# Kernel optimization log

Measured on AMD Instinct MI355X. Metric: run time of the kernel, lower is better.

## Reference

```python
import jax, jax.numpy as jnp
import numpy as np

N, IN_DIM, HID, HEADS, OUT_DIM = 50000, 128, 32, 4, 64
E, P = 800000, 500000
BN_EPS = 1e-5
NEG_SLOPE = 0.2


def setup_inputs() -> dict:
    key = jax.random.key(0)
    ks = jax.random.split(key, 16)
    inp = {
        "x": jax.random.normal(ks[0], (N, IN_DIM), jnp.float32),
        "ei": jax.random.randint(ks[1], (2, E), 0, N, jnp.int64),
        "src": jax.random.randint(ks[2], (P,), 0, N, jnp.int64),
        "dst": jax.random.randint(ks[3], (P,), 0, N, jnp.int64),
        # conv1: in_dim -> hidden, heads=4, concat
        "W1": jax.random.normal(ks[4], (IN_DIM, HEADS * HID), jnp.float32) * 0.1,
        "a1s": jax.random.normal(ks[5], (HEADS, HID), jnp.float32) * 0.1,
        "a1d": jax.random.normal(ks[6], (HEADS, HID), jnp.float32) * 0.1,
        "b1": jnp.zeros((HEADS * HID,), jnp.float32),
        "bn1_g": jnp.ones((HEADS * HID,), jnp.float32),
        "bn1_b": jnp.zeros((HEADS * HID,), jnp.float32),
        "bn1_m": jnp.zeros((HEADS * HID,), jnp.float32),
        "bn1_v": jnp.ones((HEADS * HID,), jnp.float32),
        # conv2: hidden*heads -> out_dim, heads=1, no concat
        "W2": jax.random.normal(ks[7], (HEADS * HID, OUT_DIM), jnp.float32) * 0.1,
        "a2s": jax.random.normal(ks[8], (1, OUT_DIM), jnp.float32) * 0.1,
        "a2d": jax.random.normal(ks[9], (1, OUT_DIM), jnp.float32) * 0.1,
        "b2": jnp.zeros((OUT_DIM,), jnp.float32),
        "bn2_g": jnp.ones((OUT_DIM,), jnp.float32),
        "bn2_b": jnp.zeros((OUT_DIM,), jnp.float32),
        "bn2_m": jnp.zeros((OUT_DIM,), jnp.float32),
        "bn2_v": jnp.ones((OUT_DIM,), jnp.float32),
        # head MLP: Linear(2*out_dim, out_dim) -> ELU -> Linear(out_dim, 1) -> Sigmoid
        "hW1": jax.random.normal(ks[10], (2 * OUT_DIM, OUT_DIM), jnp.float32) * 0.1,
        "hb1": jnp.zeros((OUT_DIM,), jnp.float32),
        "hW2": jax.random.normal(ks[11], (OUT_DIM, 1), jnp.float32) * 0.1,
        "hb2": jnp.zeros((1,), jnp.float32),
    }
    return inp


def gat_conv(x, e_src, e_dst, W, a_src, a_dst, bias, heads, out_dim, concat):
    # x: [N, F_in]; edges (with self-loops): e_src/e_dst [E']
    n = x.shape[0]
    h = (x @ W).reshape(n, heads, out_dim)            # [N, H, D]
    as_n = jnp.sum(h * a_src, axis=-1)                # [N, H]
    ad_n = jnp.sum(h * a_dst, axis=-1)                # [N, H]
    alpha = jax.nn.leaky_relu(as_n[e_src] + ad_n[e_dst], NEG_SLOPE)  # [E', H]
    # segment softmax over destination nodes
    m = jax.ops.segment_max(alpha, e_dst, num_segments=n)
    m = jnp.where(jnp.isfinite(m), m, 0.0)
    e = jnp.exp(alpha - m[e_dst])
    s = jax.ops.segment_sum(e, e_dst, num_segments=n)
    coef = e / (s[e_dst] + 1e-16)                     # [E', H]
    agg = jax.ops.segment_sum(h[e_src] * coef[:, :, None], e_dst, num_segments=n)
    out = agg.reshape(n, heads * out_dim) if concat else agg.mean(axis=1)
    return out + bias


def batch_norm(x, g, b, m, v):
    return (x - m) * jax.lax.rsqrt(v + BN_EPS) * g + b


def reference(x, ei, src, dst, W1, a1s, a1d, b1, bn1_g, bn1_b, bn1_m, bn1_v,
              W2, a2s, a2d, b2, bn2_g, bn2_b, bn2_m, bn2_v, hW1, hb1, hW2, hb2):
    n = x.shape[0]
    # PyG GATConv default add_self_loops=True
    loops = jnp.arange(n, dtype=ei.dtype)
    e_src = jnp.concatenate([ei[0], loops])
    e_dst = jnp.concatenate([ei[1], loops])

    z = gat_conv(x, e_src, e_dst, W1, a1s, a1d, b1, HEADS, HID, True)
    z = jax.nn.elu(batch_norm(z, bn1_g, bn1_b, bn1_m, bn1_v))
    z = gat_conv(z, e_src, e_dst, W2, a2s, a2d, b2, 1, OUT_DIM, False)
    z = jax.nn.elu(batch_norm(z, bn2_g, bn2_b, bn2_m, bn2_v))

    pair = jnp.concatenate([z[src], z[dst]], axis=1)  # [P, 2*out_dim]
    hidden = jax.nn.elu(pair @ hW1 + hb1)
    logits = hidden @ hW2 + hb2                       # [P, 1]
    return jax.nn.sigmoid(logits).squeeze(-1)
```

## Files before the change

### kernel.cpp

```cpp
#include <hip/hip_runtime.h>
#include <hip/hip_fp16.h>
#include <cmath>

#define HEADS 4
#define HID 32
#define IN_DIM 128
#define OUT_DIM 64
#define D1 (HEADS*HID)
#define NEG_SLOPE 0.2f
#define BN_EPS 1e-5f

__device__ __forceinline__ float2 h2f2(unsigned u) {
  return __half22float2(*reinterpret_cast<const __half2*>(&u));
}


__global__ void deg_count(const int* __restrict__ ei, int E, unsigned* __restrict__ deg)
{
  int e = blockIdx.x*blockDim.x + threadIdx.x;
  if (e < E) atomicAdd(&deg[ei[E + e]], 1u);
}

__global__ void tile_sum(const unsigned* __restrict__ deg, unsigned* __restrict__ part, int n)
{
  __shared__ unsigned red[256];
  int tid = threadIdx.x;
  int i = blockIdx.x*256 + tid;
  red[tid] = (i < n) ? deg[i] + 1u : 0u;
  __syncthreads();
  for (int o = 128; o >= 1; o >>= 1) {
    if (tid < o) red[tid] += red[tid + o];
    __syncthreads();
  }
  if (tid == 0) part[blockIdx.x] = red[0];
}

__global__ void part_scan(unsigned* __restrict__ part, unsigned* __restrict__ offs_n, int ntiles)
{
  __shared__ unsigned sh[256];
  int tid = threadIdx.x;
  unsigned carry = 0;
  for (int base = 0; base < ntiles; base += 256) {
    int i = base + tid;
    unsigned v = (i < ntiles) ? part[i] : 0u;
    sh[tid] = v;
    __syncthreads();
    for (int o = 1; o < 256; o <<= 1) {
      unsigned t = (tid >= o) ? sh[tid - o] : 0u;
      __syncthreads();
      sh[tid] += t;
      __syncthreads();
    }
    unsigned incl = sh[tid];
    if (i < ntiles) part[i] = carry + incl - v;
    unsigned tot = sh[255];
    __syncthreads();
    carry += tot;
  }
  if (tid == 0) offs_n[0] = carry;
}

__global__ void tile_scan_write(const unsigned* __restrict__ deg, const unsigned* __restrict__ part,
                                unsigned* __restrict__ offs, int n)
{
  __shared__ unsigned sh[256];
  int tid = threadIdx.x;
  int i = blockIdx.x*256 + tid;
  unsigned v = (i < n) ? deg[i] + 1u : 0u;
  sh[tid] = v;
  __syncthreads();
  for (int o = 1; o < 256; o <<= 1) {
    unsigned t = (tid >= o) ? sh[tid - o] : 0u;
    __syncthreads();
    sh[tid] += t;
    __syncthreads();
  }
  if (i < n) offs[i] = part[blockIdx.x] + sh[tid] - v;
}

__global__ void csr_fill(const int* __restrict__ ei, int E, int n,
                         const unsigned* __restrict__ offs, unsigned* __restrict__ cursor,
                         int* __restrict__ csr)
{
  int t = blockIdx.x*blockDim.x + threadIdx.x;
  if (t >= E + n) return;
  int s_, d_;
  if (t < E) { s_ = ei[t]; d_ = ei[E + t]; } else { s_ = d_ = t - E; }
  unsigned pos = offs[d_] + atomicAdd(&cursor[d_], 1u);
  csr[pos] = s_;
}


__global__ void gemm1(const float* __restrict__ x, const float* __restrict__ W,
                      const float* __restrict__ a_s, const float* __restrict__ a_d,
                      __half2* __restrict__ h, float* __restrict__ asn,
                      float* __restrict__ adn, int n)
{
  __shared__ float xs[8][IN_DIM];
  int base = blockIdx.x * 8;
  int tid = threadIdx.x;
  int half = tid >> 7, col = tid & 127;
  for (int idx = tid; idx < 8*IN_DIM; idx += 256) {
    int i = idx >> 7, k = idx & 127;
    int node = base + i;
    xs[i][k] = (node < n) ? x[(size_t)node*IN_DIM + k] : 0.f;
  }
  __syncthreads();
  float acc[4] = {0.f,0.f,0.f,0.f};
  for (int k = 0; k < IN_DIM; ++k) {
    float w = W[k*D1 + col];
    #pragma unroll
    for (int i = 0; i < 4; ++i) acc[i] = fmaf(xs[half*4 + i][k], w, acc[i]);
  }
  int head = col >> 5, d = col & 31;
  float vs = a_s[head*HID + d], vd = a_d[head*HID + d];
  #pragma unroll
  for (int i = 0; i < 4; ++i) {
    int node = base + half*4 + i;
    if (node >= n) break;
    float partner = __shfl_xor(acc[i], 1);
    if (!(col & 1)) h[(size_t)node*64 + (col >> 1)] = __floats2half2_rn(acc[i], partner);
    float ps = acc[i]*vs, pd = acc[i]*vd;
    #pragma unroll
    for (int m = 16; m >= 1; m >>= 1) { ps += __shfl_xor(ps, m); pd += __shfl_xor(pd, m); }
    if (d == 0) { asn[node*HEADS + head] = ps; adn[node*HEADS + head] = pd; }
  }
}

__global__ void gemm2(const float* __restrict__ z, const float* __restrict__ W,
                      const float* __restrict__ a_s, const float* __restrict__ a_d,
                      __half2* __restrict__ h2, float* __restrict__ as2,
                      float* __restrict__ ad2, int n)
{
  __shared__ float zs[4][D1];
  int base = blockIdx.x * 4;
  int tid = threadIdx.x;
  for (int idx = tid; idx < 4*D1; idx += 256) {
    int i = idx >> 7, k = idx & 127;
    int node = base + i;
    zs[i][k] = (node < n) ? z[(size_t)node*D1 + k] : 0.f;
  }
  __syncthreads();
  int i = tid >> 6, j = tid & 63;
  int node = base + i;
  float acc = 0.f;
  for (int k = 0; k < D1; ++k) acc = fmaf(zs[i][k], W[k*OUT_DIM + j], acc);
  if (node < n) {
    float partner = __shfl_xor(acc, 1);
    if (!(j & 1)) h2[(size_t)node*32 + (j >> 1)] = __floats2half2_rn(acc, partner);
    float ps = acc * a_s[j], pd = acc * a_d[j];
    #pragma unroll
    for (int m = 32; m >= 1; m >>= 1) { ps += __shfl_xor(ps, m); pd += __shfl_xor(pd, m); }
    if (j == 0) { as2[node] = ps; ad2[node] = pd; }
  }
}


__global__ void node_agg1(const int* __restrict__ csr, const unsigned* __restrict__ offs,
                          const float* __restrict__ as1, const float4* __restrict__ ad4,
                          const uint2* __restrict__ hp4, float4* __restrict__ z1out,
                          const float4* __restrict__ b1p, const float4* __restrict__ gp,
                          const float4* __restrict__ bp, const float4* __restrict__ mmp,
                          const float4* __restrict__ vvp, int n)
{
  int lane = threadIdx.x & 63;
  int node = blockIdx.x*4 + (threadIdx.x >> 6);
  if (node >= n) return;
  unsigned beg = offs[node], end = offs[node+1];
  int head = lane >> 4, sub = lane & 15;
  int h = lane >> 5, g = lane & 31;
  int lbase = (g >> 3) * 16;
  float4 advv = ad4[node];
  float adv = head==0 ? advv.x : head==1 ? advv.y : head==2 ? advv.z : advv.w;
  float a0=0.f, a1=0.f, a2=0.f, a3=0.f, s=0.f;
  for (unsigned c = beg; c < end; c += 16) {
    unsigned j = c + sub;
    bool valid = (j < end);
    int sj = valid ? csr[j] : 0;
    float al = as1[sj*HEADS + head] + adv;
    al = al > 0.f ? al : NEG_SLOPE*al;
    float w = valid ? __expf(al) : 0.f;
    float t = w;
    #pragma unroll
    for (int o = 8; o >= 1; o >>= 1) t += __shfl_xor(t, o);
    s += t;
    int cd = (int)min(16u, end - c);
    int kend = (cd + 1) & ~1;
    for (int j2 = 0; j2 < kend; j2 += 2) {
      int k = j2 + h;
      float wv = __shfl(w,  lbase + k);
      int   sv = __shfl(sj, k);
      uint2 hv = hp4[(size_t)sv*32 + g];
      float2 p0 = h2f2(hv.x), p1 = h2f2(hv.y);
      a0 = fmaf(p0.x, wv, a0); a1 = fmaf(p0.y, wv, a1);
      a2 = fmaf(p1.x, wv, a2); a3 = fmaf(p1.y, wv, a3);
    }
  }
  a0 += __shfl_xor(a0, 32); a1 += __shfl_xor(a1, 32);
  a2 += __shfl_xor(a2, 32); a3 += __shfl_xor(a3, 32);
  float sc = __shfl(s, lbase);
  float inv = 1.f / (sc + 1e-16f);
  a0 *= inv; a1 *= inv; a2 *= inv; a3 *= inv;
  if (h == 0) {
    float4 bb = b1p[g], gg = gp[g], be = bp[g], mm = mmp[g], vv = vvp[g];
    float v0 = a0 + bb.x; v0 = (v0 - mm.x) * rsqrtf(vv.x + BN_EPS) * gg.x + be.x;
    float v1 = a1 + bb.y; v1 = (v1 - mm.y) * rsqrtf(vv.y + BN_EPS) * gg.y + be.y;
    float v2 = a2 + bb.z; v2 = (v2 - mm.z) * rsqrtf(vv.z + BN_EPS) * gg.z + be.z;
    float v3 = a3 + bb.w; v3 = (v3 - mm.w) * rsqrtf(vv.w + BN_EPS) * gg.w + be.w;
    v0 = v0 > 0.f ? v0 : expm1f(v0);
    v1 = v1 > 0.f ? v1 : expm1f(v1);
    v2 = v2 > 0.f ? v2 : expm1f(v2);
    v3 = v3 > 0.f ? v3 : expm1f(v3);
    z1out[(size_t)node*32 + g] = make_float4(v0, v1, v2, v3);
  }
}

__global__ void node_agg2(const int* __restrict__ csr, const unsigned* __restrict__ offs,
                          const float* __restrict__ as2, const float* __restrict__ ad2,
                          const uint2* __restrict__ hp4,
                          const float4* __restrict__ biasp, const float4* __restrict__ gp,
                          const float4* __restrict__ bp, const float4* __restrict__ bmp,
                          const float4* __restrict__ bvp,
                          float4* __restrict__ z2out, int n)
{
  int lane = threadIdx.x & 63;
  int node = blockIdx.x*4 + (threadIdx.x >> 6);
  if (node >= n) return;
  unsigned beg = offs[node], end = offs[node+1];
  int q = lane >> 4, g = lane & 15;
  float adv = ad2[node];
  float a0=0.f, a1=0.f, a2=0.f, a3=0.f, s=0.f;
  for (unsigned c = beg; c < end; c += 64) {
    unsigned j = c + lane;
    bool valid = (j < end);
    int sj = valid ? csr[j] : 0;
    float al = as2[sj] + adv;
    al = al > 0.f ? al : NEG_SLOPE*al;
    float w = valid ? __expf(al) : 0.f;
    float t = w;
    #pragma unroll
    for (int o = 32; o >= 1; o >>= 1) t += __shfl_xor(t, o);
    s += t;
    int cd = (int)min(64u, end - c);
    int kend = (cd + 3) & ~3;
    for (int j2 = 0; j2 < kend; j2 += 4) {
      int k = j2 + q;
      float wv = __shfl(w,  k);
      int   sv = __shfl(sj, k);
      uint2 hv = hp4[(size_t)sv*16 + g];
      float2 p0 = h2f2(hv.x), p1 = h2f2(hv.y);
      a0 = fmaf(p0.x, wv, a0); a1 = fmaf(p0.y, wv, a1);
      a2 = fmaf(p1.x, wv, a2); a3 = fmaf(p1.y, wv, a3);
    }
  }
  a0 += __shfl_xor(a0, 32); a1 += __shfl_xor(a1, 32);
  a2 += __shfl_xor(a2, 32); a3 += __shfl_xor(a3, 32);
  a0 += __shfl_xor(a0, 16); a1 += __shfl_xor(a1, 16);
  a2 += __shfl_xor(a2, 16); a3 += __shfl_xor(a3, 16);
  float inv = 1.f / (s + 1e-16f);
  if (q == 0) {
    float4 bb = biasp[g], gg = gp[g], be = bp[g], mm = bmp[g], vv = bvp[g];
    float v0 = a0*inv + bb.x; v0 = (v0 - mm.x) * rsqrtf(vv.x + BN_EPS) * gg.x + be.x;
    float v1 = a1*inv + bb.y; v1 = (v1 - mm.y) * rsqrtf(vv.y + BN_EPS) * gg.y + be.y;
    float v2 = a2*inv + bb.z; v2 = (v2 - mm.z) * rsqrtf(vv.z + BN_EPS) * gg.z + be.z;
    float v3 = a3*inv + bb.w; v3 = (v3 - mm.w) * rsqrtf(vv.w + BN_EPS) * gg.w + be.w;
    v0 = v0 > 0.f ? v0 : expm1f(v0);
    v1 = v1 > 0.f ? v1 : expm1f(v1);
    v2 = v2 > 0.f ? v2 : expm1f(v2);
    v3 = v3 > 0.f ? v3 : expm1f(v3);
    z2out[(size_t)node*16 + g] = make_float4(v0, v1, v2, v3);
  }
}

__global__ void uv_prep(const float* __restrict__ z2, const float* __restrict__ hW1,
                        __half2* __restrict__ u, __half2* __restrict__ vout, int n)
{
  __shared__ float zt[64][65];
  int tid = threadIdx.x;
  int base = blockIdx.x * 64;
  for (int idx = tid; idx < 64*64; idx += 256) {
    int node = idx >> 6, k = idx & 63;
    int gn = base + node;
    zt[k][node] = (gn < n) ? z2[(size_t)gn*64 + k] : 0.f;
  }
  __syncthreads();
  int ng = tid & 7, cg = tid >> 3;
  int n0 = ng * 8;
  int c0 = (cg & 15) * 4;
  const float* wbase = hW1 + (cg >= 16 ? 64*64 : 0) + c0;
  float acc[8][4];
  #pragma unroll
  for (int i = 0; i < 8; ++i) {
    #pragma unroll
    for (int c = 0; c < 4; ++c) acc[i][c] = 0.f;
  }
  for (int k = 0; k < 64; ++k) {
    float4 w = *(const float4*)(wbase + k*64);
    float2 z01 = *(const float2*)&zt[k][n0];
    float2 z23 = *(const float2*)&zt[k][n0+2];
    float2 z45 = *(const float2*)&zt[k][n0+4];
    float2 z67 = *(const float2*)&zt[k][n0+6];
    float zz0 = z01.x, zz1 = z01.y, zz2 = z23.x, zz3 = z23.y;
    float zz4 = z45.x, zz5 = z45.y, zz6 = z67.x, zz7 = z67.y;
    acc[0][0]=fmaf(zz0,w.x,acc[0][0]); acc[0][1]=fmaf(zz0,w.y,acc[0][1]); acc[0][2]=fmaf(zz0,w.z,acc[0][2]); acc[0][3]=fmaf(zz0,w.w,acc[0][3]);
    acc[1][0]=fmaf(zz1,w.x,acc[1][0]); acc[1][1]=fmaf(zz1,w.y,acc[1][1]); acc[1][2]=fmaf(zz1,w.z,acc[1][2]); acc[1][3]=fmaf(zz1,w.w,acc[1][3]);
    acc[2][0]=fmaf(zz2,w.x,acc[2][0]); acc[2][1]=fmaf(zz2,w.y,acc[2][1]); acc[2][2]=fmaf(zz2,w.z,acc[2][2]); acc[2][3]=fmaf(zz2,w.w,acc[2][3]);
    acc[3][0]=fmaf(zz3,w.x,acc[3][0]); acc[3][1]=fmaf(zz3,w.y,acc[3][1]); acc[3][2]=fmaf(zz3,w.z,acc[3][2]); acc[3][3]=fmaf(zz3,w.w,acc[3][3]);
    acc[4][0]=fmaf(zz4,w.x,acc[4][0]); acc[4][1]=fmaf(zz4,w.y,acc[4][1]); acc[4][2]=fmaf(zz4,w.z,acc[4][2]); acc[4][3]=fmaf(zz4,w.w,acc[4][3]);
    acc[5][0]=fmaf(zz5,w.x,acc[5][0]); acc[5][1]=fmaf(zz5,w.y,acc[5][1]); acc[5][2]=fmaf(zz5,w.z,acc[5][2]); acc[5][3]=fmaf(zz5,w.w,acc[5][3]);
    acc[6][0]=fmaf(zz6,w.x,acc[6][0]); acc[6][1]=fmaf(zz6,w.y,acc[6][1]); acc[6][2]=fmaf(zz6,w.z,acc[6][2]); acc[6][3]=fmaf(zz6,w.w,acc[6][3]);
    acc[7][0]=fmaf(zz7,w.x,acc[7][0]); acc[7][1]=fmaf(zz7,w.y,acc[7][1]); acc[7][2]=fmaf(zz7,w.z,acc[7][2]); acc[7][3]=fmaf(zz7,w.w,acc[7][3]);
  }
  __half2* dst = (cg < 16) ? u : vout;
  int cq = (cg & 15) * 2;
  #pragma unroll
  for (int i = 0; i < 8; ++i) {
    int gn = base + n0 + i;
    if (gn >= n) break;
    uint2 pk;
    *reinterpret_cast<__half2*>(&pk.x) = __floats2half2_rn(acc[i][0], acc[i][1]);
    *reinterpret_cast<__half2*>(&pk.y) = __floats2half2_rn(acc[i][2], acc[i][3]);
    *reinterpret_cast<uint2*>(&dst[(size_t)gn*32 + cq]) = pk;
  }
}

__global__ void pair_score(const int* __restrict__ src, const int* __restrict__ dst,
                           const uint4* __restrict__ u4, const uint4* __restrict__ v4,
                           const float4* __restrict__ hb1, const float4* __restrict__ hW2,
                           const float* __restrict__ hb2, float* __restrict__ out, int P)
{
  int t = blockIdx.x*blockDim.x + threadIdx.x;
  int p = t >> 3, sub = t & 7;
  if (p >= P) return;
  int sp = src[p], dp = dst[p];
  uint4 ua = u4[(size_t)sp*8 + sub];
  uint4 vb = v4[(size_t)dp*8 + sub];
  float4 hbA = hb1[sub*2], hbB = hb1[sub*2+1];
  float4 w2A = hW2[sub*2], w2B = hW2[sub*2+1];
  float2 a0 = h2f2(ua.x), a1 = h2f2(ua.y), a2 = h2f2(ua.z), a3 = h2f2(ua.w);
  float2 b0 = h2f2(vb.x), b1 = h2f2(vb.y), b2 = h2f2(vb.z), b3 = h2f2(vb.w);
  float h0 = a0.x + b0.x + hbA.x; h0 = h0 > 0.f ? h0 : expm1f(h0);
  float h1 = a0.y + b0.y + hbA.y; h1 = h1 > 0.f ? h1 : expm1f(h1);
  float h2 = a1.x + b1.x + hbA.z; h2 = h2 > 0.f ? h2 : expm1f(h2);
  float h3 = a1.y + b1.y + hbA.w; h3 = h3 > 0.f ? h3 : expm1f(h3);
  float h4 = a2.x + b2.x + hbB.x; h4 = h4 > 0.f ? h4 : expm1f(h4);
  float h5 = a2.y + b2.y + hbB.y; h5 = h5 > 0.f ? h5 : expm1f(h5);
  float h6 = a3.x + b3.x + hbB.z; h6 = h6 > 0.f ? h6 : expm1f(h6);
  float h7 = a3.y + b3.y + hbB.w; h7 = h7 > 0.f ? h7 : expm1f(h7);
  float pl = h0*w2A.x + h1*w2A.y + h2*w2A.z + h3*w2A.w
           + h4*w2B.x + h5*w2B.y + h6*w2B.z + h7*w2B.w;
  pl += __shfl_xor(pl, 1);
  pl += __shfl_xor(pl, 2);
  pl += __shfl_xor(pl, 4);
  if (sub == 0) out[p] = 1.f / (1.f + __expf(-(pl + hb2[0])));
}

extern "C" void kernel_launch(void* const* d_in, const int* in_sizes, int n_in,
                              void* d_out, int out_size, void* d_ws, size_t ws_size,
                              hipStream_t stream)
{
  const float* x    = (const float*)d_in[0];
  const int*   ei   = (const int*)d_in[1];
  const int*   src  = (const int*)d_in[2];
  const int*   dst  = (const int*)d_in[3];
  const float* W1   = (const float*)d_in[4];
  const float* a1s  = (const float*)d_in[5];
  const float* a1d  = (const float*)d_in[6];
  const float* b1   = (const float*)d_in[7];
  const float* bn1g = (const float*)d_in[8];
  const float* bn1b = (const float*)d_in[9];
  const float* bn1m = (const float*)d_in[10];
  const float* bn1v = (const float*)d_in[11];
  const float* W2   = (const float*)d_in[12];
  const float* a2s  = (const float*)d_in[13];
  const float* a2d  = (const float*)d_in[14];
  const float* b2   = (const float*)d_in[15];
  const float* bn2g = (const float*)d_in[16];
  const float* bn2b = (const float*)d_in[17];
  const float* bn2m = (const float*)d_in[18];
  const float* bn2v = (const float*)d_in[19];
  const float* hW1  = (const float*)d_in[20];
  const float* hb1  = (const float*)d_in[21];
  const float* hW2  = (const float*)d_in[22];
  const float* hb2  = (const float*)d_in[23];

  const int N  = in_sizes[0] / IN_DIM;
  const int E  = in_sizes[1] / 2;
  const int P  = in_sizes[2];
  const int Ep = E + N;
  const int ntiles = (N + 255) / 256;

  float* ws = (float*)d_ws;
  float* h1   = ws;
  float* z1   = h1 + (size_t)N*D1;
  float* as1  = z1 + (size_t)N*D1;
  float* ad1  = as1 + (size_t)N*HEADS;
  float* as2  = ad1 + (size_t)N*HEADS;
  float* ad2  = as2 + N;
  unsigned* deg    = (unsigned*)(ad2 + N);
  unsigned* offs   = deg + N;
  unsigned* cursor = offs + N + 1;
  unsigned* part   = cursor + N;
  int* csr         = (int*)(part + ntiles);

  __half2* h1h = (__half2*)h1;
  __half2* h2h = (__half2*)h1;
  float*   z2  = h1 + (size_t)N*OUT_DIM;
  __half2* uh  = (__half2*)z1;
  __half2* vh  = uh + (size_t)N*32;

  hipMemsetAsync(deg,    0, (size_t)N*sizeof(unsigned), stream);
  hipMemsetAsync(cursor, 0, (size_t)N*sizeof(unsigned), stream);
  deg_count<<<(E + 255)/256, 256, 0, stream>>>(ei, E, deg);
  tile_sum<<<ntiles, 256, 0, stream>>>(deg, part, N);
  part_scan<<<1, 256, 0, stream>>>(part, offs + N, ntiles);
  tile_scan_write<<<ntiles, 256, 0, stream>>>(deg, part, offs, N);
  csr_fill<<<(Ep + 255)/256, 256, 0, stream>>>(ei, E, N, offs, cursor, csr);

  gemm1<<<(N + 7)/8, 256, 0, stream>>>(x, W1, a1s, a1d, h1h, as1, ad1, N);
  node_agg1<<<(N + 3)/4, 256, 0, stream>>>(csr, offs, as1, (const float4*)ad1,
                                           (const uint2*)h1h, (float4*)z1,
                                           (const float4*)b1, (const float4*)bn1g,
                                           (const float4*)bn1b, (const float4*)bn1m,
                                           (const float4*)bn1v, N);

  gemm2<<<(N + 3)/4, 256, 0, stream>>>(z1, W2, a2s, a2d, h2h, as2, ad2, N);
  node_agg2<<<(N + 3)/4, 256, 0, stream>>>(csr, offs, as2, ad2, (const uint2*)h2h,
                                           (const float4*)b2, (const float4*)bn2g,
                                           (const float4*)bn2b, (const float4*)bn2m,
                                           (const float4*)bn2v, (float4*)z2, N);
  uv_prep<<<(N + 63)/64, 256, 0, stream>>>(z2, hW1, uh, vh, N);

  {
    long long total = (long long)P * 8;
    int blocks = (int)((total + 255) / 256);
    pair_score<<<blocks, 256, 0, stream>>>(src, dst, (const uint4*)uh, (const uint4*)vh,
                                           (const float4*)hb1, (const float4*)hW2,
                                           hb2, (float*)d_out, P);
  }
}
```

Baseline: 335.4 us.

## Register-tile both GEMMs and fold layer-2 attention dots into aggregation

gemm1 and gemm2 are rewritten to stage 64 nodes per block in a transposed, padded shared tile, with each thread computing an 8x4 (or 8x2) register block. This gives more reuse of each weight load and LDS read than the old one-output-per-thread scheme. The layer-2 attention scalars are now computed in node_agg1 as z1 dotted with precomputed W2·a2s and W2·a2d vectors from a new prep_wa kernel, which takes the reductions out of gemm2. This reassociates the float sums and adds a tiny extra launch.

```diff
diff --git a/kernel.cpp b/kernel.cpp
--- a/kernel.cpp
+++ b/kernel.cpp
@@ -90,68 +90,127 @@
   csr[pos] = s_;
 }
 
+__global__ void prep_wa(const float* __restrict__ W2, const float* __restrict__ a2s,
+                        const float* __restrict__ a2d,
+                        float* __restrict__ wa_s, float* __restrict__ wa_d)
+{
+  int k = threadIdx.x;
+  float s = 0.f, d = 0.f;
+  for (int j = 0; j < OUT_DIM; ++j) {
+    float w = W2[k*OUT_DIM + j];
+    s = fmaf(w, a2s[j], s);
+    d = fmaf(w, a2d[j], d);
+  }
+  wa_s[k] = s; wa_d[k] = d;
+}
+
 
 __global__ void gemm1(const float* __restrict__ x, const float* __restrict__ W,
                       const float* __restrict__ a_s, const float* __restrict__ a_d,
                       __half2* __restrict__ h, float* __restrict__ asn,
                       float* __restrict__ adn, int n)
 {
-  __shared__ float xs[8][IN_DIM];
-  int base = blockIdx.x * 8;
+  __shared__ float xt[IN_DIM][65];
   int tid = threadIdx.x;
-  int half = tid >> 7, col = tid & 127;
-  for (int idx = tid; idx < 8*IN_DIM; idx += 256) {
-    int i = idx >> 7, k = idx & 127;
-    int node = base + i;
-    xs[i][k] = (node < n) ? x[(size_t)node*IN_DIM + k] : 0.f;
+  int base = blockIdx.x * 64;
+  for (int idx = tid; idx < 64*IN_DIM; idx += 256) {
+    int node = idx >> 7, k = idx & 127;
+    int gn = base + node;
+    xt[k][node] = (gn < n) ? x[(size_t)gn*IN_DIM + k] : 0.f;
   }
   __syncthreads();
-  float acc[4] = {0.f,0.f,0.f,0.f};
+  int ng = tid & 7, cg = tid >> 3;
+  int n0 = ng * 8, c0 = cg * 4;
+  float acc[8][4];
+  #pragma unroll
+  for (int i = 0; i < 8; ++i) { acc[i][0]=0.f; acc[i][1]=0.f; acc[i][2]=0.f; acc[i][3]=0.f; }
   for (int k = 0; k < IN_DIM; ++k) {
-    float w = W[k*D1 + col];
+    float4 w = *(const float4*)(W + k*D1 + c0);
+    float2 z01 = *(const float2*)&xt[k][n0];
+    float2 z23 = *(const float2*)&xt[k][n0+2];
+    float2 z45 = *(const float2*)&xt[k][n0+4];
+    float2 z67 = *(const float2*)&xt[k][n0+6];
+    float zz0=z01.x, zz1=z01.y, zz2=z23.x, zz3=z23.y, zz4=z45.x, zz5=z45.y, zz6=z67.x, zz7=z67.y;
+    acc[0][0]=fmaf(zz0,w.x,acc[0][0]); acc[0][1]=fmaf(zz0,w.y,acc[0][1]); acc[0][2]=fmaf(zz0,w.z,acc[0][2]); acc[0][3]=fmaf(zz0,w.w,acc[0][3]);
+    acc[1][0]=fmaf(zz1,w.x,acc[1][0]); acc[1][1]=fmaf(zz1,w.y,acc[1][1]); acc[1][2]=fmaf(zz1,w.z,acc[1][2]); acc[1][3]=fmaf(zz1,w.w,acc[1][3]);
+    acc[2][0]=fmaf(zz2,w.x,acc[2][0]); acc[2][1]=fmaf(zz2,w.y,acc[2][1]); acc[2][2]=fmaf(zz2,w.z,acc[2][2]); acc[2][3]=fmaf(zz2,w.w,acc[2][3]);
+    acc[3][0]=fmaf(zz3,w.x,acc[3][0]); acc[3][1]=fmaf(zz3,w.y,acc[3][1]); acc[3][2]=fmaf(zz3,w.z,acc[3][2]); acc[3][3]=fmaf(zz3,w.w,acc[3][3]);
+    acc[4][0]=fmaf(zz4,w.x,acc[4][0]); acc[4][1]=fmaf(zz4,w.y,acc[4][1]); acc[4][2]=fmaf(zz4,w.z,acc[4][2]); acc[4][3]=fmaf(zz4,w.w,acc[4][3]);
+    acc[5][0]=fmaf(zz5,w.x,acc[5][0]); acc[5][1]=fmaf(zz5,w.y,acc[5][1]); acc[5][2]=fmaf(zz5,w.z,acc[5][2]); acc[5][3]=fmaf(zz5,w.w,acc[5][3]);
+    acc[6][0]=fmaf(zz6,w.x,acc[6][0]); acc[6][1]=fmaf(zz6,w.y,acc[6][1]); acc[6][2]=fmaf(zz6,w.z,acc[6][2]); acc[6][3]=fmaf(zz6,w.w,acc[6][3]);
+    acc[7][0]=fmaf(zz7,w.x,acc[7][0]); acc[7][1]=fmaf(zz7,w.y,acc[7][1]); acc[7][2]=fmaf(zz7,w.z,acc[7][2]); acc[7][3]=fmaf(zz7,w.w,acc[7][3]);
+  }
+  #pragma unroll
+  for (int i = 0; i < 8; ++i) {
+    int gn = base + n0 + i;
+    if (gn >= n) break;
+    uint2 pk;
+    *reinterpret_cast<__half2*>(&pk.x) = __floats2half2_rn(acc[i][0], acc[i][1]);
+    *reinterpret_cast<__half2*>(&pk.y) = __floats2half2_rn(acc[i][2], acc[i][3]);
+    *reinterpret_cast<uint2*>(&h[(size_t)gn*64 + cg*2]) = pk;
+  }
+  float4 asv = *(const float4*)(a_s + c0);
+  float4 adv = *(const float4*)(a_d + c0);
+  float ps[8], pd[8];
+  #pragma unroll
+  for (int i = 0; i < 8; ++i) {
+    ps[i] = acc[i][0]*asv.x + acc[i][1]*asv.y + acc[i][2]*asv.z + acc[i][3]*asv.w;
+    pd[i] = acc[i][0]*adv.x + acc[i][1]*adv.y + acc[i][2]*adv.z + acc[i][3]*adv.w;
+  }
+  #pragma unroll
+  for (int o = 8; o <= 32; o <<= 1) {
     #pragma unroll
-    for (int i = 0; i < 4; ++i) acc[i] = fmaf(xs[half*4 + i][k], w, acc[i]);
-  }
-  int head = col >> 5, d = col & 31;
-  float vs = a_s[head*HID + d], vd = a_d[head*HID + d];
-  #pragma unroll
-  for (int i = 0; i < 4; ++i) {
-    int node = base + half*4 + i;
-    if (node >= n) break;
-    float partner = __shfl_xor(acc[i], 1);
-    if (!(col & 1)) h[(size_t)node*64 + (col >> 1)] = __floats2half2_rn(acc[i], partner);
-    float ps = acc[i]*vs, pd = acc[i]*vd;
+    for (int i = 0; i < 8; ++i) { ps[i] += __shfl_xor(ps[i], o); pd[i] += __shfl_xor(pd[i], o); }
+  }
+  if (((tid & 63) & 56) == 0) {
+    int head = tid >> 6;
     #pragma unroll
-    for (int m = 16; m >= 1; m >>= 1) { ps += __shfl_xor(ps, m); pd += __shfl_xor(pd, m); }
-    if (d == 0) { asn[node*HEADS + head] = ps; adn[node*HEADS + head] = pd; }
+    for (int i = 0; i < 8; ++i) {
+      int gn = base + n0 + i;
+      if (gn >= n) break;
+      asn[gn*HEADS + head] = ps[i];
+      adn[gn*HEADS + head] = pd[i];
+    }
   }
 }
 
 __global__ void gemm2(const float* __restrict__ z, const float* __restrict__ W,
-                      const float* __restrict__ a_s, const float* __restrict__ a_d,
-                      __half2* __restrict__ h2, float* __restrict__ as2,
-                      float* __restrict__ ad2, int n)
-{
-  __shared__ float zs[4][D1];
-  int base = blockIdx.x * 4;
+                      __half2* __restrict__ h2, int n)
+{
+  __shared__ float zt[D1][65];
   int tid = threadIdx.x;
-  for (int idx = tid; idx < 4*D1; idx += 256) {
-    int i = idx >> 7, k = idx & 127;
-    int node = base + i;
-    zs[i][k] = (node < n) ? z[(size_t)node*D1 + k] : 0.f;
+  int base = blockIdx.x * 64;
+  for (int idx = tid; idx < 64*D1; idx += 256) {
+    int node = idx >> 7, k = idx & 127;
+    int gn = base + node;
+    zt[k][node] = (gn < n) ? z[(size_t)gn*D1 + k] : 0.f;
   }
   __syncthreads();
-  int i = tid >> 6, j = tid & 63;
-  int node = base + i;
-  float acc = 0.f;
-  for (int k = 0; k < D1; ++k) acc = fmaf(zs[i][k], W[k*OUT_DIM + j], acc);
-  if (node < n) {
-    float partner = __shfl_xor(acc, 1);
-    if (!(j & 1)) h2[(size_t)node*32 + (j >> 1)] = __floats2half2_rn(acc, partner);
-    float ps = acc * a_s[j], pd = acc * a_d[j];
-    #pragma unroll
-    for (int m = 32; m >= 1; m >>= 1) { ps += __shfl_xor(ps, m); pd += __shfl_xor(pd, m); }
-    if (j == 0) { as2[node] = ps; ad2[node] = pd; }
+  int ng = tid & 7, cg = tid >> 3;
+  int n0 = ng * 8, c0 = cg * 2;
+  float a0[8], a1[8];
+  #pragma unroll
+  for (int i = 0; i < 8; ++i) { a0[i]=0.f; a1[i]=0.f; }
+  for (int k = 0; k < D1; ++k) {
+    float2 w = *(const float2*)(W + k*OUT_DIM + c0);
+    float2 z01 = *(const float2*)&zt[k][n0];
+    float2 z23 = *(const float2*)&zt[k][n0+2];
+    float2 z45 = *(const float2*)&zt[k][n0+4];
+    float2 z67 = *(const float2*)&zt[k][n0+6];
+    a0[0]=fmaf(z01.x,w.x,a0[0]); a1[0]=fmaf(z01.x,w.y,a1[0]);
+    a0[1]=fmaf(z01.y,w.x,a0[1]); a1[1]=fmaf(z01.y,w.y,a1[1]);
+    a0[2]=fmaf(z23.x,w.x,a0[2]); a1[2]=fmaf(z23.x,w.y,a1[2]);
+    a0[3]=fmaf(z23.y,w.x,a0[3]); a1[3]=fmaf(z23.y,w.y,a1[3]);
+    a0[4]=fmaf(z45.x,w.x,a0[4]); a1[4]=fmaf(z45.x,w.y,a1[4]);
+    a0[5]=fmaf(z45.y,w.x,a0[5]); a1[5]=fmaf(z45.y,w.y,a1[5]);
+    a0[6]=fmaf(z67.x,w.x,a0[6]); a1[6]=fmaf(z67.x,w.y,a1[6]);
+    a0[7]=fmaf(z67.y,w.x,a0[7]); a1[7]=fmaf(z67.y,w.y,a1[7]);
+  }
+  #pragma unroll
+  for (int i = 0; i < 8; ++i) {
+    int gn = base + n0 + i;
+    if (gn >= n) break;
+    h2[(size_t)gn*32 + cg] = __floats2half2_rn(a0[i], a1[i]);
   }
 }
 
@@ -161,7 +220,9 @@
                           const uint2* __restrict__ hp4, float4* __restrict__ z1out,
                           const float4* __restrict__ b1p, const float4* __restrict__ gp,
                           const float4* __restrict__ bp, const float4* __restrict__ mmp,
-                          const float4* __restrict__ vvp, int n)
+                          const float4* __restrict__ vvp,
+                          const float4* __restrict__ wa_s4, const float4* __restrict__ wa_d4,
+                          float* __restrict__ as2out, float* __restrict__ ad2out, int n)
 {
   int lane = threadIdx.x & 63;
   int node = blockIdx.x*4 + (threadIdx.x >> 6);
@@ -212,6 +273,12 @@
     v2 = v2 > 0.f ? v2 : expm1f(v2);
     v3 = v3 > 0.f ? v3 : expm1f(v3);
     z1out[(size_t)node*32 + g] = make_float4(v0, v1, v2, v3);
+    float4 wsv = wa_s4[g], wdv = wa_d4[g];
+    float ps = v0*wsv.x + v1*wsv.y + v2*wsv.z + v3*wsv.w;
+    float pd = v0*wdv.x + v1*wdv.y + v2*wdv.z + v3*wdv.w;
+    #pragma unroll
+    for (int o = 16; o >= 1; o >>= 1) { ps += __shfl_xor(ps, o); pd += __shfl_xor(pd, o); }
+    if (g == 0) { as2out[node] = ps; ad2out[node] = pd; }
   }
 }
 
@@ -290,18 +357,14 @@
   const float* wbase = hW1 + (cg >= 16 ? 64*64 : 0) + c0;
   float acc[8][4];
   #pragma unroll
-  for (int i = 0; i < 8; ++i) {
-    #pragma unroll
-    for (int c = 0; c < 4; ++c) acc[i][c] = 0.f;
-  }
+  for (int i = 0; i < 8; ++i) { acc[i][0]=0.f; acc[i][1]=0.f; acc[i][2]=0.f; acc[i][3]=0.f; }
   for (int k = 0; k < 64; ++k) {
     float4 w = *(const float4*)(wbase + k*64);
     float2 z01 = *(const float2*)&zt[k][n0];
     float2 z23 = *(const float2*)&zt[k][n0+2];
     float2 z45 = *(const float2*)&zt[k][n0+4];
     float2 z67 = *(const float2*)&zt[k][n0+6];
-    float zz0 = z01.x, zz1 = z01.y, zz2 = z23.x, zz3 = z23.y;
-    float zz4 = z45.x, zz5 = z45.y, zz6 = z67.x, zz7 = z67.y;
+    float zz0=z01.x, zz1=z01.y, zz2=z23.x, zz3=z23.y, zz4=z45.x, zz5=z45.y, zz6=z67.x, zz7=z67.y;
     acc[0][0]=fmaf(zz0,w.x,acc[0][0]); acc[0][1]=fmaf(zz0,w.y,acc[0][1]); acc[0][2]=fmaf(zz0,w.z,acc[0][2]); acc[0][3]=fmaf(zz0,w.w,acc[0][3]);
     acc[1][0]=fmaf(zz1,w.x,acc[1][0]); acc[1][1]=fmaf(zz1,w.y,acc[1][1]); acc[1][2]=fmaf(zz1,w.z,acc[1][2]); acc[1][3]=fmaf(zz1,w.w,acc[1][3]);
     acc[2][0]=fmaf(zz2,w.x,acc[2][0]); acc[2][1]=fmaf(zz2,w.y,acc[2][1]); acc[2][2]=fmaf(zz2,w.z,acc[2][2]); acc[2][3]=fmaf(zz2,w.w,acc[2][3]);
@@ -402,6 +465,8 @@
   unsigned* cursor = offs + N + 1;
   unsigned* part   = cursor + N;
   int* csr         = (int*)(part + ntiles);
+  float* wa_s      = (float*)(csr + Ep);
+  float* wa_d      = wa_s + D1;
 
   __half2* h1h = (__half2*)h1;
   __half2* h2h = (__half2*)h1;
@@ -411,20 +476,23 @@
 
   hipMemsetAsync(deg,    0, (size_t)N*sizeof(unsigned), stream);
   hipMemsetAsync(cursor, 0, (size_t)N*sizeof(unsigned), stream);
+  prep_wa<<<1, 128, 0, stream>>>(W2, a2s, a2d, wa_s, wa_d);
   deg_count<<<(E + 255)/256, 256, 0, stream>>>(ei, E, deg);
   tile_sum<<<ntiles, 256, 0, stream>>>(deg, part, N);
   part_scan<<<1, 256, 0, stream>>>(part, offs + N, ntiles);
   tile_scan_write<<<ntiles, 256, 0, stream>>>(deg, part, offs, N);
   csr_fill<<<(Ep + 255)/256, 256, 0, stream>>>(ei, E, N, offs, cursor, csr);
 
-  gemm1<<<(N + 7)/8, 256, 0, stream>>>(x, W1, a1s, a1d, h1h, as1, ad1, N);
+  gemm1<<<(N + 63)/64, 256, 0, stream>>>(x, W1, a1s, a1d, h1h, as1, ad1, N);
   node_agg1<<<(N + 3)/4, 256, 0, stream>>>(csr, offs, as1, (const float4*)ad1,
                                            (const uint2*)h1h, (float4*)z1,
                                            (const float4*)b1, (const float4*)bn1g,
                                            (const float4*)bn1b, (const float4*)bn1m,
-                                           (const float4*)bn1v, N);
-
-  gemm2<<<(N + 3)/4, 256, 0, stream>>>(z1, W2, a2s, a2d, h2h, as2, ad2, N);
+                                           (const float4*)bn1v,
+                                           (const float4*)wa_s, (const float4*)wa_d,
+                                           as2, ad2, N);
+
+  gemm2<<<(N + 63)/64, 256, 0, stream>>>(z1, W2, h2h, N);
   node_agg2<<<(N + 3)/4, 256, 0, stream>>>(csr, offs, as2, ad2, (const uint2*)h2h,
                                            (const float4*)b2, (const float4*)bn2g,
                                            (const float4*)bn2b, (const float4*)bn2m,
```

After: 323.6 us. -3.5%, faster.
